# Performance work log

Measured on AMD Instinct MI355X. Metric: run time of the kernel, lower is better.

The kernel has to match this reference:

```python
import jax, jax.numpy as jnp
import numpy as np

D_MODEL = 1024
H = 16
DK = D_MODEL // H
D_FC = 4096
B = 2
S = 1024
EPS = 1e-6


def setup_inputs() -> dict:
    key = jax.random.key(0)
    ks = jax.random.split(key, 8)
    sc = 1.0 / np.sqrt(D_MODEL)
    return {
        "x": jax.random.normal(ks[0], (B, S, D_MODEL), dtype=jnp.float32),
        "mask": jnp.ones((B, 1, 1, S), dtype=jnp.int32),
        "w_q": jax.random.normal(ks[1], (D_MODEL, D_MODEL), dtype=jnp.float32) * sc,
        "w_k": jax.random.normal(ks[2], (D_MODEL, D_MODEL), dtype=jnp.float32) * sc,
        "w_v": jax.random.normal(ks[3], (D_MODEL, D_MODEL), dtype=jnp.float32) * sc,
        "w_o": jax.random.normal(ks[4], (D_MODEL, D_MODEL), dtype=jnp.float32) * sc,
        "alpha1": jnp.ones((D_MODEL,), dtype=jnp.float32),
        "beta1": jnp.zeros((D_MODEL,), dtype=jnp.float32),
        "alpha2": jnp.ones((D_MODEL,), dtype=jnp.float32),
        "beta2": jnp.zeros((D_MODEL,), dtype=jnp.float32),
        "fc1_w": jax.random.normal(ks[5], (D_FC, D_MODEL), dtype=jnp.float32) * sc,
        "fc1_b": jnp.zeros((D_FC,), dtype=jnp.float32),
        "fc2_w": jax.random.normal(ks[6], (D_MODEL, D_FC), dtype=jnp.float32) * (1.0 / np.sqrt(D_FC)),
        "fc2_b": jnp.zeros((D_MODEL,), dtype=jnp.float32),
    }


def _layernorm(x, alpha, beta):
    # Matches torch: mean and std (unbiased, ddof=1), divide by (std + eps)
    mean = jnp.mean(x, axis=-1, keepdims=True)
    std = jnp.std(x, axis=-1, keepdims=True, ddof=1)
    return alpha * (x - mean) / (std + EPS) + beta


def _mha(x, mask, w_q, w_k, w_v, w_o):
    # nn.Linear(bias=False): y = x @ W.T
    q = (x @ w_q.T).reshape(B, S, H, DK).transpose(0, 2, 1, 3)  # (B,H,S,DK)
    k = (x @ w_k.T).reshape(B, S, H, DK).transpose(0, 2, 1, 3)
    v = (x @ w_v.T).reshape(B, S, H, DK).transpose(0, 2, 1, 3)
    scores = jnp.einsum('bhqd,bhkd->bhqk', q, k) / jnp.sqrt(jnp.float32(DK))
    scores = jnp.where(mask == 0, jnp.float32(-1e9), scores)
    attn = jax.nn.softmax(scores, axis=-1)  # dropout=0 (eval)
    out = jnp.einsum('bhqk,bhkd->bhqd', attn, v)  # (B,H,S,DK)
    out = out.transpose(0, 2, 1, 3).reshape(B, S, D_MODEL)
    return out @ w_o.T


def _ffn(x, fc1_w, fc1_b, fc2_w, fc2_b):
    h = jax.nn.relu(x @ fc1_w.T + fc1_b)
    return h @ fc2_w.T + fc2_b


def reference(x, mask, w_q, w_k, w_v, w_o, alpha1, beta1, alpha2, beta2,
              fc1_w, fc1_b, fc2_w, fc2_b):
    # Pre-LN residual block 1: attention
    x = x + _mha(_layernorm(x, alpha1, beta1), mask, w_q, w_k, w_v, w_o)
    # Pre-LN residual block 2: FFN
    x = x + _ffn(_layernorm(x, alpha2, beta2), fc1_w, fc1_b, fc2_w, fc2_b)
    return x
```

## Files before the change

kernel.cpp:

```cpp
#include <hip/hip_runtime.h>
#include <hip/hip_bf16.h>


typedef __bf16 bf16;
typedef __attribute__((ext_vector_type(8))) __bf16 bf16x8;
typedef __attribute__((ext_vector_type(4))) __bf16 bf16x4;
typedef __attribute__((ext_vector_type(4))) float f32x4;
typedef __attribute__((ext_vector_type(16))) float f32x16;
typedef __attribute__((ext_vector_type(4))) unsigned int u32x4;

#define NTOK 2048
#define DM   1024
#define DFC  4096
#define QKVN 3072

__device__ inline void gl_lds16(const void* g, void* l) {
    __builtin_amdgcn_global_load_lds((const __attribute__((address_space(1))) void*)g,
                                     (__attribute__((address_space(3))) void*)l, 16, 0, 0);
}

__device__ inline unsigned cvtpk_bf16(float lo, float hi) {
    unsigned r;
    asm("v_cvt_pk_bf16_f32 %0, %1, %2" : "=v"(r) : "v"(lo), "v"(hi));
    return r;
}

__device__ inline void ln_row(float4 v, const float* alpha, const float* beta,
                              bf16* outrow, int t) {
    float s  = v.x + v.y + v.z + v.w;
    float ss = v.x * v.x + v.y * v.y + v.z * v.z + v.w * v.w;
    __shared__ float red[8];
    int lane = t & 63, wv = t >> 6;
    #pragma unroll
    for (int o = 32; o > 0; o >>= 1) {
        s  += __shfl_down(s, o);
        ss += __shfl_down(ss, o);
    }
    if (lane == 0) { red[wv] = s; red[4 + wv] = ss; }
    __syncthreads();
    float S  = red[0] + red[1] + red[2] + red[3];
    float SS = red[4] + red[5] + red[6] + red[7];
    float mean = S * (1.0f / 1024.0f);
    float var  = (SS - S * mean) * (1.0f / 1023.0f);
    var = var < 0.f ? 0.f : var;
    float inv = 1.0f / (sqrtf(var) + 1e-6f);
    float4 a4 = reinterpret_cast<const float4*>(alpha)[t];
    float4 b4 = reinterpret_cast<const float4*>(beta)[t];
    bf16x4 o4;
    o4[0] = (bf16)(a4.x * (v.x - mean) * inv + b4.x);
    o4[1] = (bf16)(a4.y * (v.y - mean) * inv + b4.y);
    o4[2] = (bf16)(a4.z * (v.z - mean) * inv + b4.z);
    o4[3] = (bf16)(a4.w * (v.w - mean) * inv + b4.w);
    reinterpret_cast<bf16x4*>(outrow)[t] = o4;
}

__global__ __launch_bounds__(256) void prep_kernel(
    const float4* __restrict__ wq, const float4* __restrict__ wk,
    const float4* __restrict__ wv, const float4* __restrict__ wo,
    const float4* __restrict__ f1, const float4* __restrict__ f2,
    bf16x4* __restrict__ oqkv, bf16x4* __restrict__ oo,
    bf16x4* __restrict__ of1, bf16x4* __restrict__ of2,
    const float* __restrict__ x, const float* __restrict__ alpha1,
    const float* __restrict__ beta1, bf16* __restrict__ xn) {
    int blk = blockIdx.x;
    int t = threadIdx.x;
    if (blk < 12288) {
        int i = blk * 256 + t;
        const int Q = 262144;
        float4 v;
        bf16x4* dst;
        if (i < 3 * Q) {
            v = (i < Q) ? wq[i] : (i < 2 * Q) ? wk[i - Q] : wv[i - 2 * Q];
            dst = oqkv + i;
        } else if (i < 4 * Q) {
            v = wo[i - 3 * Q];
            dst = oo + (i - 3 * Q);
        } else if (i < 8 * Q) {
            v = f1[i - 4 * Q];
            dst = of1 + (i - 4 * Q);
        } else {
            v = f2[i - 8 * Q];
            dst = of2 + (i - 8 * Q);
        }
        bf16x4 o;
        o[0] = (bf16)v.x; o[1] = (bf16)v.y; o[2] = (bf16)v.z; o[3] = (bf16)v.w;
        *dst = o;
    } else {
        int row = blk - 12288;
        float4 v = reinterpret_cast<const float4*>(x + (size_t)row * DM)[t];
        ln_row(v, alpha1, beta1, xn + (size_t)row * DM, t);
    }
}

__global__ __launch_bounds__(256) void reduce_ln_kernel(const float* __restrict__ p,
                                                        const float* __restrict__ resid,
                                                        const float* __restrict__ alpha,
                                                        const float* __restrict__ beta,
                                                        float* __restrict__ x2,
                                                        bf16* __restrict__ xn) {
    int row = blockIdx.x, t = threadIdx.x;
    size_t i4 = (size_t)row * 256 + t;
    const size_t SL = 524288;
    float4 a = reinterpret_cast<const float4*>(p)[i4];
    float4 b = reinterpret_cast<const float4*>(p)[i4 + SL];
    float4 c = reinterpret_cast<const float4*>(p)[i4 + 2 * SL];
    float4 d = reinterpret_cast<const float4*>(p)[i4 + 3 * SL];
    float4 r = reinterpret_cast<const float4*>(resid)[i4];
    float4 v;
    v.x = a.x + b.x + c.x + d.x + r.x;
    v.y = a.y + b.y + c.y + d.y + r.y;
    v.z = a.z + b.z + c.z + d.z + r.z;
    v.w = a.w + b.w + c.w + d.w + r.w;
    reinterpret_cast<float4*>(x2)[i4] = v;
    ln_row(v, alpha, beta, xn + (size_t)row * DM, t);
}

__global__ __launch_bounds__(256) void reduce_out_kernel(const float* __restrict__ p,
                                                         const float* __restrict__ bias,
                                                         const float* __restrict__ x2,
                                                         float* __restrict__ out) {
    size_t i4 = (size_t)blockIdx.x * 256 + threadIdx.x;
    const size_t SL = 524288;
    float4 a = reinterpret_cast<const float4*>(p)[i4];
    float4 b = reinterpret_cast<const float4*>(p)[i4 + SL];
    float4 c = reinterpret_cast<const float4*>(p)[i4 + 2 * SL];
    float4 d = reinterpret_cast<const float4*>(p)[i4 + 3 * SL];
    float4 r = reinterpret_cast<const float4*>(x2)[i4];
    float4 bi = reinterpret_cast<const float4*>(bias)[i4 & 255];
    float4 o;
    o.x = a.x + b.x + c.x + d.x + r.x + bi.x;
    o.y = a.y + b.y + c.y + d.y + r.y + bi.y;
    o.z = a.z + b.z + c.z + d.z + r.z + bi.z;
    o.w = a.w + b.w + c.w + d.w + r.w + bi.w;
    reinterpret_cast<float4*>(out)[i4] = o;
}

template <int EPI>
__global__ __launch_bounds__(256) void gemm128(const bf16* __restrict__ A,
                                               const bf16* __restrict__ Bt,
                                               void* __restrict__ outp,
                                               bf16* __restrict__ vt,
                                               const float* __restrict__ bias,
                                               int M, int N, int K, int kslice,
                                               int nbx, int nby) {
    __shared__ bf16 As[2][128 * 64];
    __shared__ bf16 Bs[2][128 * 64];
    int tid = threadIdx.x;
    int lane = tid & 63, wave = tid >> 6;
    int q = lane >> 4, r = lane & 15;
    int wm = wave >> 1, wn = wave & 1;

    int lid = blockIdx.y * nbx + blockIdx.x;
    int nxp = nbx >> 3;
    int xcd = lid & 7;
    int loc = lid >> 3;
    int bx = xcd * nxp + (loc % nxp);
    int by = loc / nxp;

    int m0 = by * 128, n0 = bx * 128;
    int kbeg = blockIdx.z * kslice;
    int nit = kslice / 64;
    f32x4 acc[4][4] = {};

    int srow = tid >> 3;
    int csrc = (tid & 7) ^ (srow & 7);
    const bf16* agp = A  + (size_t)(m0 + srow) * K + kbeg + csrc * 8;
    const bf16* bgp = Bt + (size_t)(n0 + srow) * K + kbeg + csrc * 8;

    int co0 = ((q ^ (r & 7)) * 8);
    int co1 = co0 ^ 32;
    int aoff = (wm * 64 + r) * 64;
    int boff = (wn * 64 + r) * 64;

    auto stage = [&](int it, int b) {
        int k0 = it * 64;
        #pragma unroll
        for (int j = 0; j < 4; ++j) {
            gl_lds16(agp + (size_t)j * 32 * K + k0, &As[b][tid * 8 + j * 2048]);
            gl_lds16(bgp + (size_t)j * 32 * K + k0, &Bs[b][tid * 8 + j * 2048]);
        }
    };

    stage(0, 0);
    for (int it = 0; it < nit; ++it) {
        __syncthreads();
        if (it + 1 < nit) stage(it + 1, (it + 1) & 1);
        const bf16* Ab = &As[it & 1][aoff];
        const bf16* Bb = &Bs[it & 1][boff];
        #pragma unroll
        for (int half = 0; half < 2; ++half) {
            int co = half ? co1 : co0;
            bf16x8 af[4], bfv[4];
            #pragma unroll
            for (int t = 0; t < 4; ++t)
                af[t] = *reinterpret_cast<const bf16x8*>(Ab + t * 1024 + co);
            #pragma unroll
            for (int u = 0; u < 4; ++u)
                bfv[u] = *reinterpret_cast<const bf16x8*>(Bb + u * 1024 + co);
            #pragma unroll
            for (int t = 0; t < 4; ++t)
                #pragma unroll
                for (int u = 0; u < 4; ++u)
                    acc[t][u] = __builtin_amdgcn_mfma_f32_16x16x32_bf16(af[t], bfv[u], acc[t][u], 0, 0, 0);
        }
    }

    if (EPI == 2 && n0 >= 2048) {
        int bb = m0 >> 10;
        int sb = (m0 & 1023) + wm * 64 + q * 4;
        int vrow0 = bb * 1024 + (n0 - 2048) + wn * 64;
        #pragma unroll
        for (int t = 0; t < 4; ++t) {
            #pragma unroll
            for (int u = 0; u < 4; ++u) {
                bf16x4 pk;
                #pragma unroll
                for (int i = 0; i < 4; ++i) pk[i] = (bf16)acc[t][u][i];
                *reinterpret_cast<bf16x4*>(vt + (size_t)(vrow0 + u * 16 + r) * 1024 + sb + t * 16) = pk;
            }
        }
        return;
    }

    size_t zoff = (size_t)blockIdx.z * M * N;
    #pragma unroll
    for (int t = 0; t < 4; ++t) {
        #pragma unroll
        for (int u = 0; u < 4; ++u) {
            #pragma unroll
            for (int i = 0; i < 4; ++i) {
                int mm = m0 + wm * 64 + t * 16 + q * 4 + i;
                int nn = n0 + wn * 64 + u * 16 + r;
                size_t idx = (size_t)mm * N + nn;
                float v = acc[t][u][i];
                if (EPI == 1) {
                    v += bias[nn];
                    ((bf16*)outp)[idx] = (bf16)(v > 0.f ? v : 0.f);
                } else if (EPI == 2) {
                    ((bf16*)outp)[idx] = (bf16)v;
                } else {
                    ((float*)outp)[zoff + idx] = v;
                }
            }
        }
    }
}

__global__ __launch_bounds__(256) void attn_kernel(const bf16* __restrict__ qkv,
                                                   const bf16* __restrict__ Vt,
                                                   const int* __restrict__ mask,
                                                   bf16* __restrict__ out) {
    __shared__ bf16 Ks[2][4096];
    __shared__ bf16 Vs[2][4096];
    __shared__ float msk[1024];
    __shared__ float als[4][32];
    int tid = threadIdx.x;
    int lane = tid & 63, w = tid >> 6;
    int l5 = lane & 31, hi = lane >> 5;

    int id = blockIdx.x;
    int xcd = id & 7, jj = id >> 3;
    int bh = xcd * 4 + (jj >> 3);
    int qb = jj & 7;
    int b = bh >> 4, h = bh & 15;

    {
        int4 mi = reinterpret_cast<const int4*>(mask + b * 1024)[tid];
        msk[tid * 4 + 0] = mi.x ? 0.f : -1e9f;
        msk[tid * 4 + 1] = mi.y ? 0.f : -1e9f;
        msk[tid * 4 + 2] = mi.z ? 0.f : -1e9f;
        msk[tid * 4 + 3] = mi.w ? 0.f : -1e9f;
    }

    int qrow0 = qb * 128 + w * 32;
    const bf16* qp = qkv + (size_t)(b * 1024 + qrow0 + l5) * QKVN + h * 64 + hi * 8;
    bf16x8 qf[4];
    #pragma unroll
    for (int ks = 0; ks < 4; ++ks)
        qf[ks] = *reinterpret_cast<const bf16x8*>(qp + ks * 16);

    int csw = (tid & 7) ^ ((tid >> 3) & 7);
    const bf16* kg0 = qkv + (size_t)(b * 1024 + (tid >> 3)) * QKVN + 1024 + h * 64 + csw * 8;
    const bf16* kg1 = kg0 + (size_t)32 * QKVN;
    const bf16* vg0 = Vt + (size_t)((b * 16 + h) * 64 + (tid >> 3)) * 1024 + csw * 8;
    const bf16* vg1 = vg0 + 32 * 1024;
    bf16* kld = &Ks[0][tid * 8];
    bf16* vld = &Vs[0][tid * 8];

    gl_lds16(kg0, kld);
    gl_lds16(kg1, kld + 2048);
    gl_lds16(vg0, vld);
    gl_lds16(vg1, vld + 2048);

    float m_run = -1e30f, l_half = 0.f;
    f32x16 o0 = {};
    f32x16 o1 = {};

    for (int t = 0; t < 16; ++t) {
        __syncthreads();
        if (t < 15) {
            int ktn = (t + 1) * 64;
            int bo = ((t + 1) & 1) * 4096;
            gl_lds16(kg0 + (size_t)ktn * QKVN, kld + bo);
            gl_lds16(kg1 + (size_t)ktn * QKVN, kld + bo + 2048);
            gl_lds16(vg0 + ktn, vld + bo);
            gl_lds16(vg1 + ktn, vld + bo + 2048);
        }
        const bf16* Kb = Ks[t & 1];
        const bf16* Vb = Vs[t & 1];
        int kt = t * 64;

        f32x16 s0 = {}, s1 = {};
        __builtin_amdgcn_s_setprio(1);
        #pragma unroll
        for (int ks = 0; ks < 4; ++ks) {
            int ch = (((ks << 1) + hi) ^ (l5 & 7)) << 3;
            bf16x8 k0 = *reinterpret_cast<const bf16x8*>(&Kb[l5 * 64 + ch]);
            bf16x8 k1 = *reinterpret_cast<const bf16x8*>(&Kb[(32 + l5) * 64 + ch]);
            s0 = __builtin_amdgcn_mfma_f32_32x32x16_bf16(k0, qf[ks], s0, 0, 0, 0);
            s1 = __builtin_amdgcn_mfma_f32_32x32x16_bf16(k1, qf[ks], s1, 0, 0, 0);
        }
        __builtin_amdgcn_s_setprio(0);

        float p0[16], p1[16];
        float pmax = -1e30f;
        #pragma unroll
        for (int g = 0; g < 4; ++g) {
            float4 mb0 = *reinterpret_cast<const float4*>(&msk[kt + g * 8 + hi * 4]);
            float4 mb1 = *reinterpret_cast<const float4*>(&msk[kt + 32 + g * 8 + hi * 4]);
            #pragma unroll
            for (int i = 0; i < 4; ++i) {
                float mbv0 = (i == 0) ? mb0.x : (i == 1) ? mb0.y : (i == 2) ? mb0.z : mb0.w;
                float mbv1 = (i == 0) ? mb1.x : (i == 1) ? mb1.y : (i == 2) ? mb1.z : mb1.w;
                float a0 = fmaf(s0[g * 4 + i], 0.125f, mbv0);
                float a1 = fmaf(s1[g * 4 + i], 0.125f, mbv1);
                p0[g * 4 + i] = a0;
                p1[g * 4 + i] = a1;
                pmax = fmaxf(pmax, fmaxf(a0, a1));
            }
        }
        pmax = fmaxf(pmax, __shfl_xor(pmax, 32));
        float mnew = fmaxf(m_run, pmax);
        if (!__all(pmax - m_run <= 8.0f)) {
            float alpha = __expf(m_run - mnew);
            m_run = mnew;
            l_half *= alpha;
            als[w][l5] = alpha;
            #pragma unroll
            for (int g = 0; g < 4; ++g) {
                float4 av = *reinterpret_cast<const float4*>(&als[w][g * 8 + hi * 4]);
                o0[g * 4 + 0] *= av.x; o0[g * 4 + 1] *= av.y;
                o0[g * 4 + 2] *= av.z; o0[g * 4 + 3] *= av.w;
                o1[g * 4 + 0] *= av.x; o1[g * 4 + 1] *= av.y;
                o1[g * 4 + 2] *= av.z; o1[g * 4 + 3] *= av.w;
            }
        }
        float sum = 0.f;
        #pragma unroll
        for (int rg = 0; rg < 16; ++rg) {
            p0[rg] = __expf(p0[rg] - m_run);
            p1[rg] = __expf(p1[rg] - m_run);
            sum += p0[rg] + p1[rg];
        }
        l_half += sum;

        __builtin_amdgcn_s_setprio(1);
        #pragma unroll
        for (int tile = 0; tile < 2; ++tile) {
            const float* pp = tile ? p1 : p0;
            #pragma unroll
            for (int kp = 0; kp < 2; ++kp) {
                unsigned uA0 = cvtpk_bf16(pp[8 * kp + 0], pp[8 * kp + 1]);
                unsigned uA1 = cvtpk_bf16(pp[8 * kp + 2], pp[8 * kp + 3]);
                unsigned uB0 = cvtpk_bf16(pp[8 * kp + 4], pp[8 * kp + 5]);
                unsigned uB1 = cvtpk_bf16(pp[8 * kp + 6], pp[8 * kp + 7]);
                unsigned us0 = hi ? uB0 : uA0, us1 = hi ? uB1 : uA1;
                unsigned ug0 = hi ? uA0 : uB0, ug1 = hi ? uA1 : uB1;
                unsigned r0 = (unsigned)__shfl_xor((int)ug0, 32);
                unsigned r1 = (unsigned)__shfl_xor((int)ug1, 32);
                u32x4 pw_;
                pw_[0] = hi ? r0 : us0;
                pw_[1] = hi ? r1 : us1;
                pw_[2] = hi ? us0 : r0;
                pw_[3] = hi ? us1 : r1;
                bf16x8 pf = *reinterpret_cast<bf16x8*>(&pw_);
                int vch = (((tile << 2) + (kp << 1) + hi) ^ (l5 & 7)) << 3;
                bf16x8 v0 = *reinterpret_cast<const bf16x8*>(&Vb[l5 * 64 + vch]);
                bf16x8 v1 = *reinterpret_cast<const bf16x8*>(&Vb[(32 + l5) * 64 + vch]);
                o0 = __builtin_amdgcn_mfma_f32_32x32x16_bf16(pf, v0, o0, 0, 0, 0);
                o1 = __builtin_amdgcn_mfma_f32_32x32x16_bf16(pf, v1, o1, 0, 0, 0);
            }
        }
        __builtin_amdgcn_s_setprio(0);
    }

    float l_tot = l_half + __shfl_xor(l_half, 32);
    als[w][l5] = 1.0f / l_tot;
    bf16* ob = out + (size_t)(b * 1024 + qrow0) * DM + h * 64;
    #pragma unroll
    for (int g = 0; g < 4; ++g) {
        float4 iv = *reinterpret_cast<const float4*>(&als[w][g * 8 + hi * 4]);
        #pragma unroll
        for (int i = 0; i < 4; ++i) {
            float ivv = (i == 0) ? iv.x : (i == 1) ? iv.y : (i == 2) ? iv.z : iv.w;
            int qr = g * 8 + hi * 4 + i;
            ob[(size_t)qr * DM + l5]      = (bf16)(o0[g * 4 + i] * ivv);
            ob[(size_t)qr * DM + 32 + l5] = (bf16)(o1[g * 4 + i] * ivv);
        }
    }
}

extern "C" void kernel_launch(void* const* d_in, const int* in_sizes, int n_in,
                              void* d_out, int out_size, void* d_ws, size_t ws_size,
                              hipStream_t stream) {
    const float* x      = (const float*)d_in[0];
    const int*   mask   = (const int*)  d_in[1];
    const float* w_q    = (const float*)d_in[2];
    const float* w_k    = (const float*)d_in[3];
    const float* w_v    = (const float*)d_in[4];
    const float* w_o    = (const float*)d_in[5];
    const float* alpha1 = (const float*)d_in[6];
    const float* beta1  = (const float*)d_in[7];
    const float* alpha2 = (const float*)d_in[8];
    const float* beta2  = (const float*)d_in[9];
    const float* fc1_w  = (const float*)d_in[10];
    const float* fc1_b  = (const float*)d_in[11];
    const float* fc2_w  = (const float*)d_in[12];
    const float* fc2_b  = (const float*)d_in[13];
    float* out = (float*)d_out;

    char* ws = (char*)d_ws;
    const size_t MB = 1024 * 1024;
    bf16*  wqkv_b = (bf16*)(ws +  0 * MB);
    bf16*  wo_b   = (bf16*)(ws +  6 * MB);
    bf16*  f1w_b  = (bf16*)(ws +  8 * MB);
    bf16*  f2w_b  = (bf16*)(ws + 16 * MB);
    bf16*  xn     = (bf16*)(ws + 24 * MB);
    bf16*  qkvb   = (bf16*)(ws + 28 * MB);
    bf16*  vtb    = (bf16*)(ws + 40 * MB);
    bf16*  attnb  = (bf16*)(ws + 44 * MB);
    float* x2     = (float*)(ws + 48 * MB);
    float* po     = (float*)(ws + 56 * MB);
    bf16*  hb     = (bf16*)(ws + 28 * MB);
    float* pf2    = (float*)(ws + 56 * MB);

    prep_kernel<<<14336, 256, 0, stream>>>(
        (const float4*)w_q, (const float4*)w_k, (const float4*)w_v, (const float4*)w_o,
        (const float4*)fc1_w, (const float4*)fc2_w,
        (bf16x4*)wqkv_b, (bf16x4*)wo_b, (bf16x4*)f1w_b, (bf16x4*)f2w_b,
        x, alpha1, beta1, xn);

    gemm128<2><<<dim3(24, 16, 1), 256, 0, stream>>>(
        xn, wqkv_b, qkvb, vtb, nullptr, NTOK, QKVN, DM, DM, 24, 16);

    attn_kernel<<<256, 256, 0, stream>>>(qkvb, vtb, mask, attnb);

    gemm128<4><<<dim3(8, 16, 4), 256, 0, stream>>>(
        attnb, wo_b, po, nullptr, nullptr, NTOK, DM, DM, DM / 4, 8, 16);

    reduce_ln_kernel<<<NTOK, 256, 0, stream>>>(po, x, alpha2, beta2, x2, xn);

    gemm128<1><<<dim3(32, 16, 1), 256, 0, stream>>>(
        xn, f1w_b, hb, nullptr, fc1_b, NTOK, DFC, DM, DM, 32, 16);

    gemm128<4><<<dim3(8, 16, 4), 256, 0, stream>>>(
        hb, f2w_b, pf2, nullptr, nullptr, NTOK, DM, DFC, DFC / 4, 8, 16);

    reduce_out_kernel<<<2048, 256, 0, stream>>>(pf2, fc2_b, x2, out);
}
```

Before: 246.4 us.

## Move Wo/FFN weight conversion into attention kernel to overlap with attention

The prep kernel now converts only the QKV weights and runs LayerNorm1. The fp32-to-bf16 conversion of w_o, fc1 and fc2 moves into extra blocks appended to the attention launch, 2304 blocks each handling 1024 float4s. The aim is to take this bandwidth-bound conversion off the critical path before the QKV GEMM and hide it alongside the compute-bound attention blocks. The risk is that the extra blocks compete with attention for CUs and memory bandwidth, and that block scheduling order may delay the attention blocks.

Measured after the change: 239.3 us. -2.9%, faster.

```diff
diff --git a/kernel.cpp b/kernel.cpp
--- a/kernel.cpp
+++ b/kernel.cpp
@@ -56,37 +56,20 @@
 
 __global__ __launch_bounds__(256) void prep_kernel(
     const float4* __restrict__ wq, const float4* __restrict__ wk,
-    const float4* __restrict__ wv, const float4* __restrict__ wo,
-    const float4* __restrict__ f1, const float4* __restrict__ f2,
-    bf16x4* __restrict__ oqkv, bf16x4* __restrict__ oo,
-    bf16x4* __restrict__ of1, bf16x4* __restrict__ of2,
+    const float4* __restrict__ wv, bf16x4* __restrict__ oqkv,
     const float* __restrict__ x, const float* __restrict__ alpha1,
     const float* __restrict__ beta1, bf16* __restrict__ xn) {
     int blk = blockIdx.x;
     int t = threadIdx.x;
-    if (blk < 12288) {
+    if (blk < 3072) {
         int i = blk * 256 + t;
         const int Q = 262144;
-        float4 v;
-        bf16x4* dst;
-        if (i < 3 * Q) {
-            v = (i < Q) ? wq[i] : (i < 2 * Q) ? wk[i - Q] : wv[i - 2 * Q];
-            dst = oqkv + i;
-        } else if (i < 4 * Q) {
-            v = wo[i - 3 * Q];
-            dst = oo + (i - 3 * Q);
-        } else if (i < 8 * Q) {
-            v = f1[i - 4 * Q];
-            dst = of1 + (i - 4 * Q);
-        } else {
-            v = f2[i - 8 * Q];
-            dst = of2 + (i - 8 * Q);
-        }
+        float4 v = (i < Q) ? wq[i] : (i < 2 * Q) ? wk[i - Q] : wv[i - 2 * Q];
         bf16x4 o;
         o[0] = (bf16)v.x; o[1] = (bf16)v.y; o[2] = (bf16)v.z; o[3] = (bf16)v.w;
-        *dst = o;
+        oqkv[i] = o;
     } else {
-        int row = blk - 12288;
+        int row = blk - 3072;
         float4 v = reinterpret_cast<const float4*>(x + (size_t)row * DM)[t];
         ln_row(v, alpha1, beta1, xn + (size_t)row * DM, t);
     }
@@ -249,12 +232,37 @@
 __global__ __launch_bounds__(256) void attn_kernel(const bf16* __restrict__ qkv,
                                                    const bf16* __restrict__ Vt,
                                                    const int* __restrict__ mask,
-                                                   bf16* __restrict__ out) {
+                                                   bf16* __restrict__ out,
+                                                   const float4* __restrict__ cwo,
+                                                   const float4* __restrict__ cf1,
+                                                   const float4* __restrict__ cf2,
+                                                   bf16x4* __restrict__ oo,
+                                                   bf16x4* __restrict__ of1,
+                                                   bf16x4* __restrict__ of2) {
     __shared__ bf16 Ks[2][4096];
     __shared__ bf16 Vs[2][4096];
     __shared__ float msk[1024];
     __shared__ float als[4][32];
     int tid = threadIdx.x;
+
+    if (blockIdx.x >= 256) {
+        int base = (blockIdx.x - 256) * 1024;
+        const int Q = 262144;
+        #pragma unroll
+        for (int k = 0; k < 4; ++k) {
+            int i = base + k * 256 + tid;
+            float4 v;
+            bf16x4* dst;
+            if (i < Q)          { v = cwo[i];         dst = oo  + i; }
+            else if (i < 5 * Q) { v = cf1[i - Q];     dst = of1 + (i - Q); }
+            else                { v = cf2[i - 5 * Q]; dst = of2 + (i - 5 * Q); }
+            bf16x4 o;
+            o[0] = (bf16)v.x; o[1] = (bf16)v.y; o[2] = (bf16)v.z; o[3] = (bf16)v.w;
+            *dst = o;
+        }
+        return;
+    }
+
     int lane = tid & 63, w = tid >> 6;
     int l5 = lane & 31, hi = lane >> 5;
 
@@ -444,16 +452,17 @@
     bf16*  hb     = (bf16*)(ws + 28 * MB);
     float* pf2    = (float*)(ws + 56 * MB);
 
-    prep_kernel<<<14336, 256, 0, stream>>>(
-        (const float4*)w_q, (const float4*)w_k, (const float4*)w_v, (const float4*)w_o,
-        (const float4*)fc1_w, (const float4*)fc2_w,
-        (bf16x4*)wqkv_b, (bf16x4*)wo_b, (bf16x4*)f1w_b, (bf16x4*)f2w_b,
-        x, alpha1, beta1, xn);
+    prep_kernel<<<5120, 256, 0, stream>>>(
+        (const float4*)w_q, (const float4*)w_k, (const float4*)w_v,
+        (bf16x4*)wqkv_b, x, alpha1, beta1, xn);
 
     gemm128<2><<<dim3(24, 16, 1), 256, 0, stream>>>(
         xn, wqkv_b, qkvb, vtb, nullptr, NTOK, QKVN, DM, DM, 24, 16);
 
-    attn_kernel<<<256, 256, 0, stream>>>(qkvb, vtb, mask, attnb);
+    attn_kernel<<<2560, 256, 0, stream>>>(
+        qkvb, vtb, mask, attnb,
+        (const float4*)w_o, (const float4*)fc1_w, (const float4*)fc2_w,
+        (bf16x4*)wo_b, (bf16x4*)f1w_b, (bf16x4*)f2w_b);
 
     gemm128<4><<<dim3(8, 16, 4), 256, 0, stream>>>(
         attnb, wo_b, po, nullptr, nullptr, NTOK, DM, DM, DM / 4, 8, 16);
```
